# Performance work log

Measured on AMD Instinct MI355X. Metric: run time of the kernel, lower is better.

Reference implementation:

```python
import jax, jax.numpy as jnp
import numpy as np

NG, K, LEN_KEEP = 128, 32, 32  # n_groups, group_size, int(128*(1-0.75))
ENC_HEADS, DEC_HEADS = 12, 16


def _fps(xyz, init, npoint):
    # iterative farthest point sampling; xyz (B,N,3), init (B,) start indices
    B, N, _ = xyz.shape
    def step(carry, _):
        dmin, far = carry
        c = jnp.take_along_axis(xyz, far[:, None, None], axis=1)  # (B,1,3)
        dmin = jnp.minimum(dmin, jnp.sum((xyz - c) ** 2, -1))
        return (dmin, jnp.argmax(dmin, -1)), far
    _, cents = jax.lax.scan(step, (jnp.full((B, N), 1e10, xyz.dtype), init), None, length=npoint)
    return cents.T  # (B, npoint)


def _knn(xyz, cents, k):
    # squared-distance knn (same ordering as euclidean cdist + topk smallest)
    x2 = jnp.sum(xyz * xyz, -1)          # (B,N)
    c2 = jnp.sum(cents * cents, -1)      # (B,M)
    d = c2[:, :, None] + x2[:, None, :] - 2.0 * jnp.einsum('bmc,bnc->bmn', cents, xyz)
    idx = jax.lax.top_k(-d, k)[1]        # (B,M,k)
    return jax.vmap(lambda p, i: p[i])(xyz, idx)  # (B,M,k,3)


def _bn(x, g, b):
    # train-mode BatchNorm1d over (batch, spatial), channel-last x (BM,k,C)
    m = x.mean((0, 1))
    v = x.var((0, 1))
    return (x - m) * jax.lax.rsqrt(v + 1e-5) * g + b


def _ln(x, g, b):
    m = x.mean(-1, keepdims=True)
    v = ((x - m) ** 2).mean(-1, keepdims=True)
    return (x - m) * jax.lax.rsqrt(v + 1e-5) * g + b


def _layer(x, qw, qb, ow, ob, l1g, l1b, f1w, f1b, f2w, f2b, l2g, l2b, nh):
    # post-norm TransformerEncoderLayer (relu FFN, no dropout = eval mode)
    B, S, D = x.shape
    dh = D // nh
    q, k, v = jnp.split(x @ qw.T + qb, 3, axis=-1)
    q = q.reshape(B, S, nh, dh); k = k.reshape(B, S, nh, dh); v = v.reshape(B, S, nh, dh)
    att = jax.nn.softmax(jnp.einsum('bqhd,bkhd->bhqk', q, k) * (1.0 / float(np.sqrt(dh))), axis=-1)
    o = jnp.einsum('bhqk,bkhd->bqhd', att, v).reshape(B, S, D) @ ow.T + ob
    x = _ln(x + o, l1g, l1b)
    f = jax.nn.relu(x @ f1w.T + f1b) @ f2w.T + f2b
    return _ln(x + f, l2g, l2b)


def _stack(x, qw, qb, ow, ob, l1g, l1b, f1w, f1b, f2w, f2b, l2g, l2b, nh):
    for i in range(qw.shape[0]):
        x = _layer(x, qw[i], qb[i], ow[i], ob[i], l1g[i], l1b[i], f1w[i], f1b[i], f2w[i], f2b[i], l2g[i], l2b[i], nh)
    return x


def _forward(xyz, fps_init, ids_shuffle, cw1, cb1, g1, be1, cw2, cb2, g2, be2, cw3, cb3, g3, be3, pos_w, pos_b, eqw, eqb, eow, eob, el1g, el1b, ef1w, ef1b, ef2w, ef2b, el2g, el2b, dew, deb, mtok, dpw, dpb, dqw, dqb, dow, dob, dl1g, dl1b, df1w, df1b, df2w, df2b, dl2g, dl2b, prw, prb):
    B = xyz.shape[0]
    cent_idx = _fps(xyz, fps_init, NG)
    cxyz = jax.vmap(lambda p, i: p[i])(xyz, cent_idx)      # (B,NG,3)
    gn = _knn(xyz, cxyz, K) - cxyz[:, :, None, :]          # (B,NG,K,3) centered groups
    h = gn.reshape(-1, K, 3)
    h = jax.nn.relu(_bn(h @ cw1.T + cb1, g1, be1))
    h = jax.nn.relu(_bn(h @ cw2.T + cb2, g2, be2))
    h = _bn(h @ cw3.T + cb3, g3, be3)
    tokens = h.max(axis=1).reshape(B, NG, -1)              # (B,NG,768)
    x = tokens + cxyz @ pos_w.T + pos_b
    ids_restore = jnp.argsort(ids_shuffle, axis=1)
    xk = jnp.take_along_axis(x, ids_shuffle[:, :LEN_KEEP, None], axis=1)
    mask = jnp.ones((B, NG), xyz.dtype).at[:, :LEN_KEEP].set(0.0)
    mask = jnp.take_along_axis(mask, ids_restore, axis=1)
    lat = _stack(xk, eqw, eqb, eow, eob, el1g, el1b, ef1w, ef1b, ef2w, ef2b, el2g, el2b, ENC_HEADS)
    y = lat @ dew.T + deb
    mt = jnp.broadcast_to(mtok, (B, NG - LEN_KEEP, mtok.shape[0]))
    y_ = jnp.take_along_axis(jnp.concatenate([y, mt], axis=1), ids_restore[:, :, None], axis=1)
    yd = y_ + cxyz @ dpw.T + dpb
    dec = _stack(yd, dqw, dqb, dow, dob, dl1g, dl1b, df1w, df1b, df2w, df2b, dl2g, dl2b, DEC_HEADS)
    pred = dec @ prw.T + prb                               # (B,NG,K*3)
    target = gn.reshape(B, NG, -1)                         # same FPS seed -> same centroids in loss branch
    l = ((pred - target) ** 2).mean(-1)
    loss = (l * mask).sum() / mask.sum()
    return loss, pred, mask


def setup_inputs():
    ks = iter(jax.random.split(jax.random.key(0), 64))
    def W(*shape):
        return jax.random.normal(next(ks), shape, jnp.float32) * 0.02
    B, N, D, DD, Le, Ld = 32, 8192, 768, 512, 12, 8
    d = {}
    d['xyz'] = jax.random.normal(next(ks), (B, N, 3), jnp.float32)
    d['fps_init'] = jax.random.randint(next(ks), (B,), 0, N)
    d['ids_shuffle'] = jnp.argsort(jax.random.uniform(next(ks), (B, NG)), axis=1)
    d['cw1'], d['cb1'], d['g1'], d['be1'] = W(64, 3), jnp.zeros(64), jnp.ones(64), jnp.zeros(64)
    d['cw2'], d['cb2'], d['g2'], d['be2'] = W(128, 64), jnp.zeros(128), jnp.ones(128), jnp.zeros(128)
    d['cw3'], d['cb3'], d['g3'], d['be3'] = W(D, 128), jnp.zeros(D), jnp.ones(D), jnp.zeros(D)
    d['pos_w'], d['pos_b'] = W(D, 3), jnp.zeros(D)
    d['eqw'], d['eqb'] = W(Le, 3 * D, D), jnp.zeros((Le, 3 * D))
    d['eow'], d['eob'] = W(Le, D, D), jnp.zeros((Le, D))
    d['el1g'], d['el1b'] = jnp.ones((Le, D)), jnp.zeros((Le, D))
    d['ef1w'], d['ef1b'] = W(Le, 4 * D, D), jnp.zeros((Le, 4 * D))
    d['ef2w'], d['ef2b'] = W(Le, D, 4 * D), jnp.zeros((Le, D))
    d['el2g'], d['el2b'] = jnp.ones((Le, D)), jnp.zeros((Le, D))
    d['dew'], d['deb'] = W(DD, D), jnp.zeros(DD)
    d['mtok'] = jnp.zeros(DD)
    d['dpw'], d['dpb'] = W(DD, 3), jnp.zeros(DD)
    d['dqw'], d['dqb'] = W(Ld, 3 * DD, DD), jnp.zeros((Ld, 3 * DD))
    d['dow'], d['dob'] = W(Ld, DD, DD), jnp.zeros((Ld, DD))
    d['dl1g'], d['dl1b'] = jnp.ones((Ld, DD)), jnp.zeros((Ld, DD))
    d['df1w'], d['df1b'] = W(Ld, 4 * DD, DD), jnp.zeros((Ld, 4 * DD))
    d['df2w'], d['df2b'] = W(Ld, DD, 4 * DD), jnp.zeros((Ld, DD))
    d['dl2g'], d['dl2b'] = jnp.ones((Ld, DD)), jnp.zeros((Ld, DD))
    d['prw'], d['prb'] = W(K * 3, DD), jnp.zeros(K * 3)
    return d


def reference(xyz, fps_init, ids_shuffle, cw1, cb1, g1, be1, cw2, cb2, g2, be2, cw3, cb3, g3, be3, pos_w, pos_b, eqw, eqb, eow, eob, el1g, el1b, ef1w, ef1b, ef2w, ef2b, el2g, el2b, dew, deb, mtok, dpw, dpb, dqw, dqb, dow, dob, dl1g, dl1b, df1w, df1b, df2w, df2b, dl2g, dl2b, prw, prb):
    return _forward(xyz, fps_init, ids_shuffle, cw1, cb1, g1, be1, cw2, cb2, g2, be2, cw3, cb3, g3, be3, pos_w, pos_b, eqw, eqb, eow, eob, el1g, el1b, ef1w, ef1b, ef2w, ef2b, el2g, el2b, dew, deb, mtok, dpw, dpb, dqw, dqb, dow, dob, dl1g, dl1b, df1w, df1b, df2w, df2b, dl2g, dl2b, prw, prb)
```

## Files before the change

### kernel.cpp

```cpp
#include <hip/hip_runtime.h>
#include <cmath>

#define BB 32
#define NPTS 8192
#define NG 128
#define KNB 32
#define LK 32
#define DE 768
#define DD 512
#define NLE 12
#define NLD 8

typedef __bf16 bf16x8 __attribute__((ext_vector_type(8)));
typedef float  f32x4  __attribute__((ext_vector_type(4)));
typedef unsigned long long u64;

#define WAITV(N) asm volatile("s_waitcnt vmcnt(" #N ")" ::: "memory")

static __device__ __forceinline__ bf16x8 pack8(float4 a, float4 b) {
    bf16x8 h;
    h[0] = (__bf16)a.x; h[1] = (__bf16)a.y; h[2] = (__bf16)a.z; h[3] = (__bf16)a.w;
    h[4] = (__bf16)b.x; h[5] = (__bf16)b.y; h[6] = (__bf16)b.z; h[7] = (__bf16)b.w;
    return h;
}

static __device__ __forceinline__ void gload16(const __bf16* g, __bf16* l) {
    __builtin_amdgcn_global_load_lds(
        (const __attribute__((address_space(1))) void*)g,
        (__attribute__((address_space(3))) void*)l,
        16, 0, 0);
}

static __device__ __forceinline__ unsigned fkey(float f) {
    unsigned u = __float_as_uint(f);
    return ((int)u < 0) ? ~u : (u | 0x80000000u);
}

__global__ __launch_bounds__(256, 1) void fps_kernel(
    const float* __restrict__ xyz, const int* __restrict__ init,
    float* __restrict__ cxyz)
{
#pragma clang fp contract(off)
    const int b = blockIdx.x;
    const float* P = xyz + (size_t)b * NPTS * 3;
    __shared__ float pxs[NPTS], pys[NPTS], pzs[NPTS];
    __shared__ u64 red[2][4];
    const int tid = threadIdx.x;
    float x[32], y[32], z[32], dmin[32];
    #pragma unroll
    for (int k = 0; k < 32; ++k) {
        int n = tid + (k << 8);
        float xx = P[n * 3 + 0], yy = P[n * 3 + 1], zz = P[n * 3 + 2];
        x[k] = xx; y[k] = yy; z[k] = zz;
        pxs[n] = xx; pys[n] = yy; pzs[n] = zz;
        dmin[k] = 1e10f;
    }
    int far = init[b];
    __syncthreads();
    for (int t = 0; t < NG; ++t) {
        float cx = pxs[far], cy = pys[far], cz = pzs[far];
        if (tid == 0) {
            cxyz[(b * NG + t) * 3 + 0] = cx;
            cxyz[(b * NG + t) * 3 + 1] = cy;
            cxyz[(b * NG + t) * 3 + 2] = cz;
        }
        u64 key = 0ull;
        #pragma unroll
        for (int k = 0; k < 32; ++k) {
            float dx = x[k] - cx, dy = y[k] - cy, dz = z[k] - cz;
            float d = dx * dx + dy * dy + dz * dz;
            float dm = dmin[k];
            if (d < dm) dm = d;
            dmin[k] = dm;
            u64 kk = ((u64)__float_as_uint(dm) << 32) | (unsigned)(8191 - (tid + (k << 8)));
            if (kk > key) key = kk;
        }
        #pragma unroll
        for (int d = 32; d >= 1; d >>= 1) {
            u64 k2 = __shfl_down(key, d);
            if (k2 > key) key = k2;
        }
        if ((tid & 63) == 0) red[t & 1][tid >> 6] = key;
        __syncthreads();
        u64 kb = red[t & 1][0];
        #pragma unroll
        for (int w = 1; w < 4; ++w) {
            u64 k2 = red[t & 1][w];
            if (k2 > kb) kb = k2;
        }
        far = 8191 - (int)(kb & 0xFFFFFFFFu);
    }
}

__global__ __launch_bounds__(256) void knn_kernel(
    const float* __restrict__ xyz, const float* __restrict__ cxyz,
    float* __restrict__ gn)
{
#pragma clang fp contract(off)
    const int bm = blockIdx.x;
    const int b = bm / NG;
    const float* P = xyz + (size_t)b * NPTS * 3;
    __shared__ u64 cand[128];
    __shared__ int order[KNB];
    const int tid = threadIdx.x;
    const int wv = tid >> 6, lane = tid & 63;
    const float cx = cxyz[bm * 3 + 0], cy = cxyz[bm * 3 + 1], cz = cxyz[bm * 3 + 2];
    const float c2 = cx * cx + cy * cy + cz * cz;
    float d[32];
    float best = 1e31f; int bi = 1 << 30;
    #pragma unroll
    for (int j = 0; j < 32; ++j) {
        int n = tid + (j << 8);
        float x = P[n * 3 + 0], y = P[n * 3 + 1], z = P[n * 3 + 2];
        float x2 = x * x + y * y + z * z;
        float dt = cx * x + cy * y + cz * z;
        float v = (c2 + x2) - 2.0f * dt;
        d[j] = v;
        if (v < best) { best = v; bi = n; }
    }
    for (int r = 0; r < KNB; ++r) {
        float v = best; int i = bi;
        #pragma unroll
        for (int dd = 32; dd >= 1; dd >>= 1) {
            float v2 = __shfl_down(v, dd); int i2 = __shfl_down(i, dd);
            if (v2 < v || (v2 == v && i2 < i)) { v = v2; i = i2; }
        }
        v = __shfl(v, 0); i = __shfl(i, 0);
        if (lane == 0)
            cand[wv * 32 + r] = ((u64)fkey(v) << 32) | (unsigned)i;
        if ((i & 255) == tid) {
            int sj = i >> 8;
            best = 1e31f; bi = 1 << 30;
            #pragma unroll
            for (int j = 0; j < 32; ++j) {
                float vv = (j == sj) ? 1e30f : d[j];
                d[j] = vv;
                if (vv < best) { best = vv; bi = tid + (j << 8); }
            }
        }
    }
    __syncthreads();
    if (wv == 0) {
        u64 my0 = cand[lane], my1 = cand[lane + 64];
        int r0 = 0, r1 = 0;
        #pragma unroll 16
        for (int j = 0; j < 128; ++j) {
            u64 k = cand[j];
            r0 += (k < my0); r1 += (k < my1);
        }
        if (r0 < KNB) order[r0] = (int)(my0 & 0xFFFFFFFFu);
        if (r1 < KNB) order[r1] = (int)(my1 & 0xFFFFFFFFu);
    }
    __syncthreads();
    if (tid < KNB) {
        int n = order[tid];
        gn[((size_t)bm * KNB + tid) * 3 + 0] = P[n * 3 + 0] - cx;
        gn[((size_t)bm * KNB + tid) * 3 + 1] = P[n * 3 + 1] - cy;
        gn[((size_t)bm * KNB + tid) * 3 + 2] = P[n * 3 + 2] - cz;
    }
}

__global__ void cvt_bf16_kernel(const float* __restrict__ src, __bf16* __restrict__ dst, int n8)
{
    int i = blockIdx.x * 256 + threadIdx.x;
    if (i >= n8) return;
    const float4* p = (const float4*)(src + (size_t)i * 8);
    *(bf16x8*)(dst + (size_t)i * 8) = pack8(p[0], p[1]);
}

__global__ void embed1_kernel(const float* __restrict__ gn, const float* __restrict__ w,
                              const float* __restrict__ bias, float* __restrict__ h1)
{
    int i = blockIdx.x * 256 + threadIdx.x;
    if (i >= 131072 * 64) return;
    int r = i >> 6, c = i & 63;
    const float* p = gn + (size_t)r * 3;
    h1[i] = p[0] * w[c * 3 + 0] + p[1] * w[c * 3 + 1] + p[2] * w[c * 3 + 2] + bias[c];
}

template <int C>
__global__ __launch_bounds__(256) void colstats_kernel(const float* __restrict__ X,
                                                       double* __restrict__ st, int Mrows)
{
    constexpr int RL = 256 / C;
    const int c = threadIdx.x % C;
    const int rl = threadIdx.x / C;
    double s = 0.0, s2 = 0.0;
    int rows_per_block = (Mrows + gridDim.x - 1) / gridDim.x;
    int r0 = blockIdx.x * rows_per_block;
    int r1 = min(r0 + rows_per_block, Mrows);
    for (int r = r0 + rl; r < r1; r += RL) {
        float v = X[(size_t)r * C + c];
        s += v; s2 += (double)v * v;
    }
    __shared__ double sh[2][256];
    sh[0][threadIdx.x] = s; sh[1][threadIdx.x] = s2;
    __syncthreads();
    if (rl == 0) {
        for (int j = 1; j < RL; ++j) { s += sh[0][j * C + c]; s2 += sh[1][j * C + c]; }
        atomicAdd(&st[c], s);
        atomicAdd(&st[C + c], s2);
    }
}

__global__ void bn_finalize(const double* __restrict__ st, const float* __restrict__ g,
                            const float* __restrict__ be, float* __restrict__ sc,
                            float* __restrict__ shb, int C)
{
    int c = blockIdx.x * 64 + threadIdx.x;
    if (c >= C) return;
    double m = st[c] / 131072.0;
    double var = st[C + c] / 131072.0 - m * m;
    if (var < 0.0) var = 0.0;
    float rs = rsqrtf((float)var + 1e-5f);
    sc[c] = rs * g[c];
    shb[c] = be[c] - (float)m * rs * g[c];
}

__global__ void bn_apply_bf16(const float* __restrict__ x, const float* __restrict__ sc,
                              const float* __restrict__ shb, __bf16* __restrict__ y,
                              int total, int C)
{
    int i = blockIdx.x * 256 + threadIdx.x;
    if (i >= total) return;
    int c = i % C;
    float v = x[i] * sc[c] + shb[c];
    v = fmaxf(v, 0.0f);
    y[i] = (__bf16)v;
}

template <int BM, int WM, int WN, int DEPTH>
__global__ __launch_bounds__(256) void gemm_bf16(
    const __bf16* __restrict__ A, const __bf16* __restrict__ W,
    const float* __restrict__ bias, float* __restrict__ Cf, __bf16* __restrict__ Cb,
    int M, int N, int K, int Kc, int relu)
{
    constexpr int MR = BM / WM / 16;
    constexpr int NR = 128 / WN / 16;
    constexpr int CA = BM * 8 / 256;
    __shared__ __bf16 As[DEPTH][BM * 64];
    __shared__ __bf16 Ws[DEPTH][128 * 64];
    const int tid = threadIdx.x;
    const int lane = tid & 63;
    const int wave = tid >> 6;
    const int wm = wave / WN, wn = wave % WN;
    const int m0 = blockIdx.y * BM, n0 = blockIdx.x * 128;
    const int kb = blockIdx.z * Kc;

    f32x4 acc[MR][NR] = {};

    auto stage = [&](int buf, int kt) {
        #pragma unroll
        for (int j = 0; j < CA; ++j) {
            int cb = j * 256 + (wave << 6);
            int c  = cb + lane;
            int row = c >> 3;
            int kcs = (c & 7) ^ (row & 7);
            gload16(A + (size_t)(m0 + row) * K + kb + kt + kcs * 8, &As[buf][cb * 8]);
        }
        #pragma unroll
        for (int j = 0; j < 4; ++j) {
            int cb = j * 256 + (wave << 6);
            int c  = cb + lane;
            int row = c >> 3;
            int kcs = (c & 7) ^ (row & 7);
            gload16(W + (size_t)(n0 + row) * K + kb + kt + kcs * 8, &Ws[buf][cb * 8]);
        }
    };
    auto compute = [&](int buf) {
        #pragma unroll
        for (int ks = 0; ks < 2; ++ks) {
            bf16x8 af[MR], bfr[NR];
            int kc = ks * 4 + (lane >> 4);
            #pragma unroll
            for (int i = 0; i < MR; ++i) {
                int rowA = wm * (BM / WM) + i * 16 + (lane & 15);
                af[i] = *(bf16x8*)&As[buf][rowA * 64 + ((kc ^ (rowA & 7)) * 8)];
            }
            #pragma unroll
            for (int j = 0; j < NR; ++j) {
                int rowB = wn * (128 / WN) + j * 16 + (lane & 15);
                bfr[j] = *(bf16x8*)&Ws[buf][rowB * 64 + ((kc ^ (rowB & 7)) * 8)];
            }
            #pragma unroll
            for (int i = 0; i < MR; ++i)
                #pragma unroll
                for (int j = 0; j < NR; ++j)
                    acc[i][j] = __builtin_amdgcn_mfma_f32_16x16x32_bf16(af[i], bfr[j], acc[i][j], 0, 0, 0);
        }
    };

    const int nt = Kc >> 6;
    if constexpr (DEPTH == 3) {
        stage(0, 0);
        if (nt > 1) stage(1, 64);
        for (int t = 0; t < nt; ++t) {
            if (t < nt - 1) { if constexpr (BM == 64) WAITV(6); else WAITV(8); }
            else            WAITV(0);
            __syncthreads();
            if (t + 2 < nt) stage((t + 2) % 3, (t + 2) << 6);
            compute(t % 3);
        }
    } else {
        stage(0, 0);
        if (nt > 1) stage(1, 64);
        for (int t = 0; t < nt; ++t) {
            if (t < nt - 1) { if constexpr (BM == 64) WAITV(6); else WAITV(8); }
            else            WAITV(0);
            __syncthreads();
            compute(t % 2);
            if (t + 2 <= nt - 1) {
                __syncthreads();
                stage(t % 2, (t + 2) << 6);
            }
        }
    }

    float* Co = Cf ? Cf + (size_t)blockIdx.z * M * N : nullptr;
    #pragma unroll
    for (int j = 0; j < NR; ++j) {
        int col = n0 + wn * (128 / WN) + j * 16 + (lane & 15);
        if (col >= N) continue;
        float bv = (blockIdx.z == 0) ? bias[col] : 0.0f;
        #pragma unroll
        for (int i = 0; i < MR; ++i) {
            #pragma unroll
            for (int r = 0; r < 4; ++r) {
                int rowm = m0 + wm * (BM / WM) + i * 16 + (lane >> 4) * 4 + r;
                float v = acc[i][j][r] + bv;
                if (relu) v = fmaxf(v, 0.0f);
                if (Co) Co[(size_t)rowm * N + col] = v;
                if (Cb) Cb[(size_t)rowm * N + col] = (__bf16)v;
            }
        }
    }
}

__global__ __launch_bounds__(256) void embed3_mfma(
    const __bf16* __restrict__ A, const __bf16* __restrict__ W,
    const float* __restrict__ cb3,
    float* __restrict__ gmax, float* __restrict__ gmin, double* __restrict__ st3)
{
    __shared__ __bf16 As[2][128 * 64];
    __shared__ __bf16 Ws[2][128 * 64];
    const int tid = threadIdx.x;
    const int lane = tid & 63;
    const int wave = tid >> 6;
    const int wm = wave >> 1, wn = wave & 1;
    const int m0 = blockIdx.y * 128, n0 = blockIdx.x * 128;
    const int K = 128;

    f32x4 acc[4][4] = {};

    auto stage = [&](int buf, int kt) {
        #pragma unroll
        for (int j = 0; j < 4; ++j) {
            int cb = j * 256 + (wave << 6);
            int c  = cb + lane;
            int row = c >> 3;
            int kcs = (c & 7) ^ (row & 7);
            gload16(A + (size_t)(m0 + row) * K + kt + kcs * 8, &As[buf][cb * 8]);
            gload16(W + (size_t)(n0 + row) * K + kt + kcs * 8, &Ws[buf][cb * 8]);
        }
    };
    auto compute = [&](int buf) {
        #pragma unroll
        for (int ks = 0; ks < 2; ++ks) {
            bf16x8 af[4], bfr[4];
            int kc = ks * 4 + (lane >> 4);
            #pragma unroll
            for (int i = 0; i < 4; ++i) {
                int rowA = wm * 64 + i * 16 + (lane & 15);
                af[i] = *(bf16x8*)&As[buf][rowA * 64 + ((kc ^ (rowA & 7)) * 8)];
                int rowB = wn * 64 + i * 16 + (lane & 15);
                bfr[i] = *(bf16x8*)&Ws[buf][rowB * 64 + ((kc ^ (rowB & 7)) * 8)];
            }
            #pragma unroll
            for (int i = 0; i < 4; ++i)
                #pragma unroll
                for (int j = 0; j < 4; ++j)
                    acc[i][j] = __builtin_amdgcn_mfma_f32_16x16x32_bf16(af[i], bfr[j], acc[i][j], 0, 0, 0);
        }
    };

    stage(0, 0);
    stage(1, 64);
    WAITV(8);
    __syncthreads();
    compute(0);
    WAITV(0);
    __syncthreads();
    compute(1);

    #pragma unroll
    for (int j = 0; j < 4; ++j) {
        int col = n0 + wn * 64 + j * 16 + (lane & 15);
        float bv = cb3[col];
        float stot = 0.0f, s2tot = 0.0f;
        #pragma unroll
        for (int gi = 0; gi < 2; ++gi) {
            float mx = -1e30f, mn = 1e30f, s = 0.0f, s2 = 0.0f;
            #pragma unroll
            for (int ii = 0; ii < 2; ++ii) {
                f32x4 a = acc[gi * 2 + ii][j];
                #pragma unroll
                for (int r = 0; r < 4; ++r) {
                    float v = a[r] + bv;
                    mx = fmaxf(mx, v); mn = fminf(mn, v);
                    s += v; s2 += v * v;
                }
            }
            #pragma unroll
            for (int d = 16; d < 64; d <<= 1) {
                mx = fmaxf(mx, __shfl_xor(mx, d));
                mn = fminf(mn, __shfl_xor(mn, d));
                s  += __shfl_xor(s, d);
                s2 += __shfl_xor(s2, d);
            }
            stot += s; s2tot += s2;
            if (lane < 16) {
                int g = (m0 >> 5) + wm * 2 + gi;
                gmax[(size_t)g * 768 + col] = mx;
                gmin[(size_t)g * 768 + col] = mn;
            }
        }
        if (lane < 16) {
            double* stp = st3 + (size_t)(blockIdx.y & 31) * 1536;
            atomicAdd(&stp[col], (double)stot);
            atomicAdd(&stp[768 + col], (double)s2tot);
        }
    }
}

__global__ void bn3_finalize(const double* __restrict__ st3, const float* __restrict__ g,
                             const float* __restrict__ be, float* __restrict__ a3,
                             float* __restrict__ c3)
{
    int c = blockIdx.x * 256 + threadIdx.x;
    if (c >= 768) return;
    double s = 0.0, s2 = 0.0;
    for (int p = 0; p < 32; ++p) { s += st3[(size_t)p * 1536 + c]; s2 += st3[(size_t)p * 1536 + 768 + c]; }
    double m = s / 131072.0;
    double var = s2 / 131072.0 - m * m;
    if (var < 0.0) var = 0.0;
    float rs = rsqrtf((float)var + 1e-5f);
    a3[c] = rs * g[c];
    c3[c] = be[c] - (float)m * rs * g[c];
}

__global__ void tokens_pos(const float* __restrict__ gmax, const float* __restrict__ gmin,
                           const float* __restrict__ a3, const float* __restrict__ c3,
                           const float* __restrict__ cxyz, const float* __restrict__ posw,
                           const float* __restrict__ posb, float* __restrict__ x)
{
    int i = blockIdx.x * 256 + threadIdx.x;
    if (i >= 4096 * 768) return;
    int c = i % 768, g = i / 768;
    float a = a3[c];
    float tok = (a >= 0.0f ? a * gmax[i] : a * gmin[i]) + c3[c];
    float px = cxyz[g * 3 + 0], py = cxyz[g * 3 + 1], pz = cxyz[g * 3 + 2];
    x[i] = tok + px * posw[c * 3 + 0] + py * posw[c * 3 + 1] + pz * posw[c * 3 + 2] + posb[c];
}

__global__ void restore_kernel(const int* __restrict__ shuffle, int* __restrict__ restore,
                               float* __restrict__ maskv)
{
    int j = blockIdx.x * 256 + threadIdx.x;
    if (j >= BB * NG) return;
    int b = j / NG, p = j % NG;
    int dst = b * NG + shuffle[j];
    restore[dst] = p;
    maskv[dst] = (p < LK) ? 0.0f : 1.0f;
}

__global__ void gather_xk(const float* __restrict__ xfull, const int* __restrict__ shuffle,
                          float* __restrict__ xe, __bf16* __restrict__ xeb)
{
    int i = blockIdx.x * 256 + threadIdx.x;
    if (i >= BB * LK * DE) return;
    int c = i % DE;
    int s = (i / DE) % LK;
    int b = i / (DE * LK);
    float v = xfull[((size_t)b * NG + shuffle[b * NG + s]) * DE + c];
    xe[i] = v;
    xeb[i] = (__bf16)v;
}

__global__ void yd_build(const float* __restrict__ ykp, const int* __restrict__ restore,
                         const float* __restrict__ mtok, const float* __restrict__ cxyz,
                         const float* __restrict__ dpw, const float* __restrict__ dpb,
                         float* __restrict__ xd, __bf16* __restrict__ xdb)
{
    const size_t PS = (size_t)1024 * DD;
    int i = blockIdx.x * 256 + threadIdx.x;
    if (i >= BB * NG * DD) return;
    int c = i % DD;
    int g = i / DD;
    int b = g / NG;
    int r = restore[g];
    float base;
    if (r < LK) {
        size_t o = (size_t)(b * LK + r) * DD + c;
        base = ykp[o] + ykp[PS + o] + ykp[2 * PS + o] + ykp[3 * PS + o];
    } else {
        base = mtok[c];
    }
    float px = cxyz[g * 3 + 0], py = cxyz[g * 3 + 1], pz = cxyz[g * 3 + 2];
    float v = base + px * dpw[c * 3 + 0] + py * dpw[c * 3 + 1] + pz * dpw[c * 3 + 2] + dpb[c];
    xd[i] = v;
    xdb[i] = (__bf16)v;
}

template <int S, int DH, int QT, int NH>
__global__ __launch_bounds__(256) void attn_kernel(const float* __restrict__ qkv,
                                                   __bf16* __restrict__ o, float scale)
{
    constexpr int D = NH * DH;
    constexpr int NT = S / QT;
    constexpr int DH4 = DH / 4;
    constexpr int KW = DH + 4;
    constexpr int PS = S + 4;
    constexpr int CH = S / 8;
    __shared__ float Ks[S][KW];
    __shared__ float Vs[S][KW];
    __shared__ float Qs[QT][KW];
    __shared__ float Pb[QT][PS];
    const int t = blockIdx.x % NT;
    const int h = (blockIdx.x / NT) % NH;
    const int b = blockIdx.x / (NT * NH);
    const float* base = qkv + (size_t)b * S * 3 * D + h * DH;
    for (int i = threadIdx.x; i < S * DH4; i += 256) {
        int s = i / DH4, d4 = (i % DH4) * 4;
        *(float4*)&Ks[s][d4] = *(const float4*)&base[(size_t)s * 3 * D + D + d4];
        *(float4*)&Vs[s][d4] = *(const float4*)&base[(size_t)s * 3 * D + 2 * D + d4];
    }
    for (int i = threadIdx.x; i < QT * DH4; i += 256) {
        int qi = i / DH4, d4 = (i % DH4) * 4;
        *(float4*)&Qs[qi][d4] = *(const float4*)&base[(size_t)(t * QT + qi) * 3 * D + d4];
    }
    __syncthreads();
    for (int i = threadIdx.x; i < QT * S; i += 256) {
        int qi = i / S, s = i % S;
        float acc = 0.0f;
        #pragma unroll
        for (int d4 = 0; d4 < DH; d4 += 4) {
            float4 q = *(float4*)&Qs[qi][d4];
            float4 k = *(float4*)&Ks[s][d4];
            acc += q.x * k.x + q.y * k.y + q.z * k.z + q.w * k.w;
        }
        Pb[qi][s] = acc * scale;
    }
    __syncthreads();
    {
        int qi = threadIdx.x >> 3;
        int sub = threadIdx.x & 7;
        float mx = -1e30f;
        #pragma unroll
        for (int j = 0; j < CH; ++j) mx = fmaxf(mx, Pb[qi][sub * CH + j]);
        #pragma unroll
        for (int d = 4; d >= 1; d >>= 1) mx = fmaxf(mx, __shfl_xor(mx, d));
        float sum = 0.0f;
        #pragma unroll
        for (int j = 0; j < CH; ++j) {
            float e = expf(Pb[qi][sub * CH + j] - mx);
            Pb[qi][sub * CH + j] = e;
            sum += e;
        }
        #pragma unroll
        for (int d = 4; d >= 1; d >>= 1) sum += __shfl_xor(sum, d);
        float inv = 1.0f / sum;
        #pragma unroll
        for (int j = 0; j < CH; ++j) Pb[qi][sub * CH + j] *= inv;
    }
    __syncthreads();
    __bf16* ob = o + (size_t)b * S * D + h * DH;
    for (int i = threadIdx.x; i < QT * DH4; i += 256) {
        int qi = i / DH4, d4 = (i % DH4) * 4;
        float4 acc = {0, 0, 0, 0};
        for (int s = 0; s < S; ++s) {
            float p = Pb[qi][s];
            float4 v = *(float4*)&Vs[s][d4];
            acc.x += p * v.x; acc.y += p * v.y; acc.z += p * v.z; acc.w += p * v.w;
        }
        __bf16 o4[4] = {(__bf16)acc.x, (__bf16)acc.y, (__bf16)acc.z, (__bf16)acc.w};
        *(ushort4*)&ob[(size_t)(t * QT + qi) * D + d4] = *(ushort4*)o4;
    }
}

template <int D, int SK>
__global__ __launch_bounds__(256) void ln_res(float* __restrict__ x, const float* __restrict__ part,
                                              size_t pstride,
                                              const float* __restrict__ g, const float* __restrict__ b,
                                              __bf16* __restrict__ xb)
{
    constexpr int J = D / 256;
    __shared__ float pr[2][4];
    const size_t off = (size_t)blockIdx.x * D;
    const int tid = threadIdx.x;
    float vals[J];
    float s = 0.0f, s2 = 0.0f;
    #pragma unroll
    for (int j = 0; j < J; ++j) {
        int i = tid + j * 256;
        float v = x[off + i];
        #pragma unroll
        for (int sk = 0; sk < SK; ++sk) v += part[(size_t)sk * pstride + off + i];
        vals[j] = v; s += v; s2 += v * v;
    }
    #pragma unroll
    for (int d = 32; d >= 1; d >>= 1) { s += __shfl_down(s, d); s2 += __shfl_down(s2, d); }
    if ((tid & 63) == 0) { pr[0][tid >> 6] = s; pr[1][tid >> 6] = s2; }
    __syncthreads();
    float st = pr[0][0] + pr[0][1] + pr[0][2] + pr[0][3];
    float s2t = pr[1][0] + pr[1][1] + pr[1][2] + pr[1][3];
    float m = st / D;
    float var = s2t / D - m * m;
    if (var < 0.0f) var = 0.0f;
    float rs = rsqrtf(var + 1e-5f);
    #pragma unroll
    for (int j = 0; j < J; ++j) {
        int i = tid + j * 256;
        float v = (vals[j] - m) * rs * g[i] + b[i];
        x[off + i] = v;
        xb[off + i] = (__bf16)v;
    }
}

__global__ __launch_bounds__(128) void loss_l(const float* __restrict__ pred,
                                              const float* __restrict__ target,
                                              const float* __restrict__ maskv,
                                              float* __restrict__ lm)
{
    const int g = blockIdx.x;
    __shared__ float red[128];
    int t = threadIdx.x;
    float s = 0.0f;
    if (t < 96) {
        float d = pred[(size_t)g * 96 + t] - target[(size_t)g * 96 + t];
        s = d * d;
    }
    red[t] = s; __syncthreads();
    for (int st = 64; st > 0; st >>= 1) { if (t < st) red[t] += red[t + st]; __syncthreads(); }
    if (t == 0) lm[g] = (red[0] / 96.0f) * maskv[g];
}

__global__ __launch_bounds__(1024) void loss_final(const float* __restrict__ lm,
                                                   const float* __restrict__ maskv,
                                                   float* __restrict__ out)
{
    __shared__ float r1[1024], r2[1024];
    int t = threadIdx.x;
    float a = 0.0f, b = 0.0f;
    for (int i = t; i < BB * NG; i += 1024) { a += lm[i]; b += maskv[i]; }
    r1[t] = a; r2[t] = b; __syncthreads();
    for (int st = 512; st > 0; st >>= 1) { if (t < st) { r1[t] += r1[t + st]; r2[t] += r2[t + st]; } __syncthreads(); }
    if (t == 0) out[0] = r1[0] / r2[0];
}

extern "C" void kernel_launch(void* const* d_in, const int* in_sizes, int n_in,
                              void* d_out, int out_size, void* d_ws, size_t ws_size,
                              hipStream_t stream)
{
    (void)in_sizes; (void)n_in; (void)out_size; (void)ws_size;
    const float* xyz        = (const float*)d_in[0];
    const int*   fps_init   = (const int*)d_in[1];
    const int*   ids_shuf   = (const int*)d_in[2];
    const float* cw1 = (const float*)d_in[3];  const float* cb1 = (const float*)d_in[4];
    const float* g1  = (const float*)d_in[5];  const float* be1 = (const float*)d_in[6];
    const float* cw2 = (const float*)d_in[7];  const float* cb2 = (const float*)d_in[8];
    const float* g2  = (const float*)d_in[9];  const float* be2 = (const float*)d_in[10];
    const float* cw3 = (const float*)d_in[11]; const float* cb3 = (const float*)d_in[12];
    const float* g3  = (const float*)d_in[13]; const float* be3 = (const float*)d_in[14];
    const float* posw = (const float*)d_in[15]; const float* posb = (const float*)d_in[16];
    const float* eqw = (const float*)d_in[17]; const float* eqb = (const float*)d_in[18];
    const float* eow = (const float*)d_in[19]; const float* eob = (const float*)d_in[20];
    const float* el1g = (const float*)d_in[21]; const float* el1b = (const float*)d_in[22];
    const float* ef1w = (const float*)d_in[23]; const float* ef1b = (const float*)d_in[24];
    const float* ef2w = (const float*)d_in[25]; const float* ef2b = (const float*)d_in[26];
    const float* el2g = (const float*)d_in[27]; const float* el2b = (const float*)d_in[28];
    const float* dew = (const float*)d_in[29]; const float* deb = (const float*)d_in[30];
    const float* mtok = (const float*)d_in[31];
    const float* dpw = (const float*)d_in[32]; const float* dpb = (const float*)d_in[33];
    const float* dqw = (const float*)d_in[34]; const float* dqb = (const float*)d_in[35];
    const float* dow = (const float*)d_in[36]; const float* dob = (const float*)d_in[37];
    const float* dl1g = (const float*)d_in[38]; const float* dl1b = (const float*)d_in[39];
    const float* df1w = (const float*)d_in[40]; const float* df1b = (const float*)d_in[41];
    const float* df2w = (const float*)d_in[42]; const float* df2b = (const float*)d_in[43];
    const float* dl2g = (const float*)d_in[44]; const float* dl2b = (const float*)d_in[45];
    const float* prw = (const float*)d_in[46]; const float* prb = (const float*)d_in[47];
    float* out = (float*)d_out;
    float* pred = out + 1;
    float* maskv = out + 1 + (size_t)BB * NG * KNB * 3;

    char* ws = (char*)d_ws;
    size_t off = 0;
    auto alloc = [&](size_t bytes) -> void* {
        void* p = ws + off;
        off = (off + bytes + 255) & ~(size_t)255;
        return p;
    };
    double* st1 = (double*)alloc(128 * 8);
    double* st2 = (double*)alloc(256 * 8);
    double* st3 = (double*)alloc((size_t)32 * 1536 * 8);
    float* sc1 = (float*)alloc(64 * 4);  float* sh1 = (float*)alloc(64 * 4);
    float* sc2 = (float*)alloc(128 * 4); float* sh2 = (float*)alloc(128 * 4);
    float* a3 = (float*)alloc(768 * 4);  float* c3 = (float*)alloc(768 * 4);
    int* restore = (int*)alloc(4096 * 4);
    float* cxyz = (float*)alloc(12288 * 4);
    float* gn   = (float*)alloc((size_t)393216 * 4);
    __bf16* cw2b = (__bf16*)alloc((size_t)128 * 64 * 2);
    __bf16* cw3b = (__bf16*)alloc((size_t)768 * 128 * 2);
    float* xfull = (float*)alloc((size_t)4096 * 768 * 4);
    float* xe    = (float*)alloc((size_t)1024 * 768 * 4);
    __bf16* xeb  = (__bf16*)alloc((size_t)1024 * 768 * 2);
    float* qkve  = (float*)alloc((size_t)1024 * 2304 * 4);
    __bf16* oeb  = (__bf16*)alloc((size_t)1024 * 768 * 2);
    __bf16* fe1b = (__bf16*)alloc((size_t)1024 * 3072 * 2);
    float* xd    = (float*)alloc((size_t)4096 * 512 * 4);
    __bf16* xdb  = (__bf16*)alloc((size_t)4096 * 512 * 2);
    float* qkvd  = (float*)alloc((size_t)4096 * 1536 * 4);
    __bf16* odb  = (__bf16*)alloc((size_t)4096 * 512 * 2);
    __bf16* fd1b = (__bf16*)alloc((size_t)4096 * 2048 * 2);
    float* lm    = (float*)alloc(4096 * 4);

    __bf16* eqwb  = (__bf16*)alloc((size_t)NLE * 3 * DE * DE * 2);
    __bf16* eowb  = (__bf16*)alloc((size_t)NLE * DE * DE * 2);
    __bf16* ef1wb = (__bf16*)alloc((size_t)NLE * 4 * DE * DE * 2);
    __bf16* ef2wb = (__bf16*)alloc((size_t)NLE * 4 * DE * DE * 2);
    __bf16* dewb  = (__bf16*)alloc((size_t)DD * DE * 2);
    __bf16* dqwb  = (__bf16*)alloc((size_t)NLD * 3 * DD * DD * 2);
    __bf16* dowb  = (__bf16*)alloc((size_t)NLD * DD * DD * 2);
    __bf16* df1wb = (__bf16*)alloc((size_t)NLD * 4 * DD * DD * 2);
    __bf16* df2wb = (__bf16*)alloc((size_t)NLD * 4 * DD * DD * 2);
    __bf16* prwb  = (__bf16*)alloc((size_t)128 * 512 * 2);

    char* U = (char*)eqwb;
    float*  h1   = (float*)U;
    __bf16* h1b  = (__bf16*)(U + (size_t)33554432);
    float*  h2   = (float*)(U + (size_t)50331648);
    __bf16* h2b  = (__bf16*)(U + (size_t)117440512);
    float*  gmax = (float*)(U + (size_t)150994944);
    float*  gmin = (float*)(U + (size_t)163577856);

    size_t stats_bytes = (size_t)((char*)st3 + (size_t)32 * 1536 * 8 - (char*)st1);
    hipMemsetAsync((void*)st1, 0, stats_bytes, stream);

    auto cvt = [&](const float* src, __bf16* dst, size_t n) {
        int n8 = (int)(n / 8);
        cvt_bf16_kernel<<<(n8 + 255) / 256, 256, 0, stream>>>(src, dst, n8);
    };
    auto gemm = [&](const __bf16* A, const __bf16* Wt, const float* bias,
                    float* Cf, __bf16* Cb, int M, int N, int K, int relu) {
        int nb128 = ((N + 127) / 128) * (M / 128);
        if (nb128 < 256) {
            dim3 grid((N + 127) / 128, M / 64, 1);
            gemm_bf16<64, 1, 4, 3><<<grid, 256, 0, stream>>>(A, Wt, bias, Cf, Cb, M, N, K, K, relu);
        } else {
            dim3 grid((N + 127) / 128, M / 128, 1);
            gemm_bf16<128, 2, 2, 2><<<grid, 256, 0, stream>>>(A, Wt, bias, Cf, Cb, M, N, K, K, relu);
        }
    };
    auto gemmSK = [&](const __bf16* A, const __bf16* Wt, const float* bias,
                      float* Cf, int M, int N, int K, int SK) {
        dim3 grid((N + 127) / 128, M / 64, SK);
        gemm_bf16<64, 1, 4, 3><<<grid, 256, 0, stream>>>(A, Wt, bias, Cf, nullptr, M, N, K, K / SK, 0);
    };

    cvt(cw2, cw2b, 128 * 64);
    cvt(cw3, cw3b, 768 * 128);

    fps_kernel<<<BB, 256, 0, stream>>>(xyz, fps_init, cxyz);
    knn_kernel<<<BB * NG, 256, 0, stream>>>(xyz, cxyz, gn);

    embed1_kernel<<<(131072 * 64 + 255) / 256, 256, 0, stream>>>(gn, cw1, cb1, h1);
    colstats_kernel<64><<<256, 256, 0, stream>>>(h1, st1, 131072);
    bn_finalize<<<1, 64, 0, stream>>>(st1, g1, be1, sc1, sh1, 64);
    bn_apply_bf16<<<(131072 * 64 + 255) / 256, 256, 0, stream>>>(h1, sc1, sh1, h1b, 131072 * 64, 64);
    gemm(h1b, cw2b, cb2, h2, nullptr, 131072, 128, 64, 0);
    colstats_kernel<128><<<256, 256, 0, stream>>>(h2, st2, 131072);
    bn_finalize<<<2, 64, 0, stream>>>(st2, g2, be2, sc2, sh2, 128);
    bn_apply_bf16<<<(131072 * 128 + 255) / 256, 256, 0, stream>>>(h2, sc2, sh2, h2b, 131072 * 128, 128);
    embed3_mfma<<<dim3(6, 1024), 256, 0, stream>>>(h2b, cw3b, cb3, gmax, gmin, st3);
    bn3_finalize<<<3, 256, 0, stream>>>(st3, g3, be3, a3, c3);
    tokens_pos<<<(4096 * 768 + 255) / 256, 256, 0, stream>>>(gmax, gmin, a3, c3, cxyz, posw, posb, xfull);

    restore_kernel<<<16, 256, 0, stream>>>(ids_shuf, restore, maskv);
    gather_xk<<<(BB * LK * DE + 255) / 256, 256, 0, stream>>>(xfull, ids_shuf, xe, xeb);

    cvt(eqw,  eqwb,  (size_t)NLE * 3 * DE * DE);
    cvt(eow,  eowb,  (size_t)NLE * DE * DE);
    cvt(ef1w, ef1wb, (size_t)NLE * 4 * DE * DE);
    cvt(ef2w, ef2wb, (size_t)NLE * 4 * DE * DE);
    cvt(dew,  dewb,  (size_t)DD * DE);
    cvt(dqw,  dqwb,  (size_t)NLD * 3 * DD * DD);
    cvt(dow,  dowb,  (size_t)NLD * DD * DD);
    cvt(df1w, df1wb, (size_t)NLD * 4 * DD * DD);
    cvt(df2w, df2wb, (size_t)NLD * 4 * DD * DD);
    cvt(prw,  prwb,  (size_t)96 * 512);
    hipMemsetAsync((void*)(prwb + (size_t)96 * 512), 0, (size_t)32 * 512 * 2, stream);

    const size_t PSE = (size_t)1024 * DE;
    const size_t PSD = (size_t)4096 * DD;

    for (int l = 0; l < NLE; ++l) {
        gemm(xeb, eqwb + (size_t)l * 3 * DE * DE, eqb + (size_t)l * 3 * DE, qkve, nullptr, 1024, 3 * DE, DE, 0);
        attn_kernel<LK, 64, 32, 12><<<BB * 12, 256, 0, stream>>>(qkve, oeb, 0.125f);
        gemmSK(oeb, eowb + (size_t)l * DE * DE, eob + (size_t)l * DE, xfull, 1024, DE, DE, 4);
        ln_res<DE, 4><<<BB * LK, 256, 0, stream>>>(xe, xfull, PSE, el1g + (size_t)l * DE, el1b + (size_t)l * DE, xeb);
        gemm(xeb, ef1wb + (size_t)l * 4 * DE * DE, ef1b + (size_t)l * 4 * DE, nullptr, fe1b, 1024, 4 * DE, DE, 1);
        gemmSK(fe1b, ef2wb + (size_t)l * DE * 4 * DE, ef2b + (size_t)l * DE, xfull, 1024, DE, 4 * DE, 4);
        ln_res<DE, 4><<<BB * LK, 256, 0, stream>>>(xe, xfull, PSE, el2g + (size_t)l * DE, el2b + (size_t)l * DE, xeb);
    }

    gemmSK(xeb, dewb, deb, qkve, 1024, DD, DE, 4);
    yd_build<<<(BB * NG * DD + 255) / 256, 256, 0, stream>>>(qkve, restore, mtok, cxyz, dpw, dpb, xd, xdb);

    const float dsc = (float)(1.0 / sqrt(32.0));
    for (int l = 0; l < NLD; ++l) {
        gemm(xdb, dqwb + (size_t)l * 3 * DD * DD, dqb + (size_t)l * 3 * DD, qkvd, nullptr, 4096, 3 * DD, DD, 0);
        attn_kernel<NG, 32, 32, 16><<<BB * 16 * (NG / 32), 256, 0, stream>>>(qkvd, odb, dsc);
        gemmSK(odb, dowb + (size_t)l * DD * DD, dob + (size_t)l * DD, qkvd, 4096, DD, DD, 2);
        ln_res<DD, 2><<<BB * NG, 256, 0, stream>>>(xd, qkvd, PSD, dl1g + (size_t)l * DD, dl1b + (size_t)l * DD, xdb);
        gemm(xdb, df1wb + (size_t)l * 4 * DD * DD, df1b + (size_t)l * 4 * DD, nullptr, fd1b, 4096, 4 * DD, DD, 1);
        gemmSK(fd1b, df2wb + (size_t)l * DD * 4 * DD, df2b + (size_t)l * DD, qkvd, 4096, DD, 4 * DD, 2);
        ln_res<DD, 2><<<BB * NG, 256, 0, stream>>>(xd, qkvd, PSD, dl2g + (size_t)l * DD, dl2b + (size_t)l * DD, xdb);
    }

    gemm(xdb, prwb, prb, pred, nullptr, 4096, 96, 512, 0);
    loss_l<<<BB * NG, 128, 0, stream>>>(pred, gn, maskv, lm);
    loss_final<<<1, 1024, 0, stream>>>(lm, maskv, out);
}
```

Baseline: 2.779 ms.

## Replace iterative kNN selection with threshold filter plus rank sort; batch weight casts

The kNN kernel no longer runs 32 rounds of wavefront argmin. Each wave bitonic-sorts its per-thread minima to get the 32nd smallest as a threshold, and all candidates at or below the tightest wave threshold are compacted into shared memory and rank-sorted. If more than 512 candidates pass, it falls back to a block-wide iterative selection. The ten separate fp32-to-bf16 weight conversion launches are also merged into one segmented kernel, which cuts launch overhead but adds a per-thread segment lookup.

```diff
diff --git a/kernel.cpp b/kernel.cpp
--- a/kernel.cpp
+++ b/kernel.cpp
@@ -100,14 +100,16 @@
     const int bm = blockIdx.x;
     const int b = bm / NG;
     const float* P = xyz + (size_t)b * NPTS * 3;
-    __shared__ u64 cand[128];
+    __shared__ u64 cand[512];
+    __shared__ u64 tmins[4];
+    __shared__ int wcnt[4];
     __shared__ int order[KNB];
     const int tid = threadIdx.x;
     const int wv = tid >> 6, lane = tid & 63;
     const float cx = cxyz[bm * 3 + 0], cy = cxyz[bm * 3 + 1], cz = cxyz[bm * 3 + 2];
     const float c2 = cx * cx + cy * cy + cz * cz;
-    float d[32];
-    float best = 1e31f; int bi = 1 << 30;
+    unsigned fk[32];
+    float bestf = 1e31f; int bi = 1 << 30;
     #pragma unroll
     for (int j = 0; j < 32; ++j) {
         int n = tid + (j << 8);
@@ -115,43 +117,99 @@
         float x2 = x * x + y * y + z * z;
         float dt = cx * x + cy * y + cz * z;
         float v = (c2 + x2) - 2.0f * dt;
-        d[j] = v;
-        if (v < best) { best = v; bi = n; }
-    }
-    for (int r = 0; r < KNB; ++r) {
-        float v = best; int i = bi;
-        #pragma unroll
-        for (int dd = 32; dd >= 1; dd >>= 1) {
-            float v2 = __shfl_down(v, dd); int i2 = __shfl_down(i, dd);
-            if (v2 < v || (v2 == v && i2 < i)) { v = v2; i = i2; }
-        }
-        v = __shfl(v, 0); i = __shfl(i, 0);
-        if (lane == 0)
-            cand[wv * 32 + r] = ((u64)fkey(v) << 32) | (unsigned)i;
-        if ((i & 255) == tid) {
-            int sj = i >> 8;
-            best = 1e31f; bi = 1 << 30;
-            #pragma unroll
-            for (int j = 0; j < 32; ++j) {
-                float vv = (j == sj) ? 1e30f : d[j];
-                d[j] = vv;
-                if (vv < best) { best = vv; bi = tid + (j << 8); }
-            }
-        }
+        fk[j] = fkey(v);
+        if (v < bestf) { bestf = v; bi = n; }
+    }
+    u64 mk = ((u64)fkey(bestf) << 32) | (unsigned)bi;
+    {
+        u64 v = mk;
+        #pragma unroll
+        for (int k = 2; k <= 64; k <<= 1) {
+            #pragma unroll
+            for (int j = k >> 1; j > 0; j >>= 1) {
+                u64 o = __shfl_xor(v, j);
+                bool up = ((lane & k) == 0);
+                bool lower = ((lane & j) == 0);
+                u64 mn = (v < o) ? v : o;
+                u64 mx = (v < o) ? o : v;
+                v = (up == lower) ? mn : mx;
+            }
+        }
+        u64 Tw = __shfl(v, 31);
+        if (lane == 0) tmins[wv] = Tw;
     }
     __syncthreads();
-    if (wv == 0) {
-        u64 my0 = cand[lane], my1 = cand[lane + 64];
-        int r0 = 0, r1 = 0;
-        #pragma unroll 16
-        for (int j = 0; j < 128; ++j) {
-            u64 k = cand[j];
-            r0 += (k < my0); r1 += (k < my1);
-        }
-        if (r0 < KNB) order[r0] = (int)(my0 & 0xFFFFFFFFu);
-        if (r1 < KNB) order[r1] = (int)(my1 & 0xFFFFFFFFu);
-    }
+    u64 T = tmins[0];
+    #pragma unroll
+    for (int w = 1; w < 4; ++w) { u64 k2 = tmins[w]; if (k2 < T) T = k2; }
+    int c = 0;
+    #pragma unroll
+    for (int j = 0; j < 32; ++j) {
+        u64 key = ((u64)fk[j] << 32) | (unsigned)(tid + (j << 8));
+        c += (key <= T) ? 1 : 0;
+    }
+    int s = c;
+    #pragma unroll
+    for (int d = 1; d < 64; d <<= 1) {
+        int t2 = __shfl_up(s, d);
+        if (lane >= d) s += t2;
+    }
+    int excl = s - c;
+    if (lane == 63) wcnt[wv] = s;
     __syncthreads();
+    int base = 0;
+    for (int w = 0; w < wv; ++w) base += wcnt[w];
+    int etot = wcnt[0] + wcnt[1] + wcnt[2] + wcnt[3];
+
+    if (etot <= 512) {
+        int pos = base + excl;
+        #pragma unroll
+        for (int j = 0; j < 32; ++j) {
+            u64 key = ((u64)fk[j] << 32) | (unsigned)(tid + (j << 8));
+            if (key <= T) cand[pos++] = key;
+        }
+        __syncthreads();
+        for (int si = tid; si < etot; si += 256) {
+            u64 my = cand[si];
+            int r = 0;
+            for (int j2 = 0; j2 < etot; ++j2) r += (cand[j2] < my) ? 1 : 0;
+            if (r < KNB) order[r] = (int)(my & 0xFFFFFFFFu);
+        }
+        __syncthreads();
+    } else {
+        u64 bk = ~0ull;
+        #pragma unroll
+        for (int j = 0; j < 32; ++j) {
+            u64 key = ((u64)fk[j] << 32) | (unsigned)(tid + (j << 8));
+            if (key < bk) bk = key;
+        }
+        for (int r = 0; r < KNB; ++r) {
+            u64 kk = bk;
+            #pragma unroll
+            for (int dd = 32; dd >= 1; dd >>= 1) {
+                u64 k2 = __shfl_down(kk, dd);
+                if (k2 < kk) kk = k2;
+            }
+            if (lane == 0) cand[(r & 1) * 4 + wv] = kk;
+            __syncthreads();
+            u64 kb = cand[(r & 1) * 4 + 0];
+            #pragma unroll
+            for (int w = 1; w < 4; ++w) { u64 k2 = cand[(r & 1) * 4 + w]; if (k2 < kb) kb = k2; }
+            if (tid == 0) order[r] = (int)(kb & 0xFFFFFFFFu);
+            if ((int)(kb & 255u) == tid) {
+                int sj = (int)((kb & 0xFFFFFFFFu) >> 8);
+                #pragma unroll
+                for (int j = 0; j < 32; ++j) if (j == sj) fk[j] = 0xFFFFFFFFu;
+                bk = ~0ull;
+                #pragma unroll
+                for (int j = 0; j < 32; ++j) {
+                    u64 key = ((u64)fk[j] << 32) | (unsigned)(tid + (j << 8));
+                    if (key < bk) bk = key;
+                }
+            }
+            __syncthreads();
+        }
+    }
     if (tid < KNB) {
         int n = order[tid];
         gn[((size_t)bm * KNB + tid) * 3 + 0] = P[n * 3 + 0] - cx;
@@ -166,6 +224,23 @@
     if (i >= n8) return;
     const float4* p = (const float4*)(src + (size_t)i * 8);
     *(bf16x8*)(dst + (size_t)i * 8) = pack8(p[0], p[1]);
+}
+
+struct CvtTab {
+    const float* src[10];
+    __bf16* dst[10];
+    int cum[11];
+};
+__global__ void cvt_multi_kernel(CvtTab t)
+{
+    int i = blockIdx.x * 256 + threadIdx.x;
+    if (i >= t.cum[10]) return;
+    int seg = 0;
+    #pragma unroll
+    for (int k = 1; k < 10; ++k) seg += (i >= t.cum[k]) ? 1 : 0;
+    int local = i - t.cum[seg];
+    const float4* p = (const float4*)(t.src[seg] + (size_t)local * 8);
+    *(bf16x8*)(t.dst[seg] + (size_t)local * 8) = pack8(p[0], p[1]);
 }
 
 __global__ void embed1_kernel(const float* __restrict__ gn, const float* __restrict__ w,
@@ -787,17 +862,28 @@
     restore_kernel<<<16, 256, 0, stream>>>(ids_shuf, restore, maskv);
     gather_xk<<<(BB * LK * DE + 255) / 256, 256, 0, stream>>>(xfull, ids_shuf, xe, xeb);
 
-    cvt(eqw,  eqwb,  (size_t)NLE * 3 * DE * DE);
-    cvt(eow,  eowb,  (size_t)NLE * DE * DE);
-    cvt(ef1w, ef1wb, (size_t)NLE * 4 * DE * DE);
-    cvt(ef2w, ef2wb, (size_t)NLE * 4 * DE * DE);
-    cvt(dew,  dewb,  (size_t)DD * DE);
-    cvt(dqw,  dqwb,  (size_t)NLD * 3 * DD * DD);
-    cvt(dow,  dowb,  (size_t)NLD * DD * DD);
-    cvt(df1w, df1wb, (size_t)NLD * 4 * DD * DD);
-    cvt(df2w, df2wb, (size_t)NLD * 4 * DD * DD);
-    cvt(prw,  prwb,  (size_t)96 * 512);
-    hipMemsetAsync((void*)(prwb + (size_t)96 * 512), 0, (size_t)32 * 512 * 2, stream);
+    {
+        CvtTab t;
+        const float* srcs[10] = {eqw, eow, ef1w, ef2w, dew, dqw, dow, df1w, df2w, prw};
+        __bf16* dsts[10] = {eqwb, eowb, ef1wb, ef2wb, dewb, dqwb, dowb, df1wb, df2wb, prwb};
+        size_t ns[10] = {
+            (size_t)NLE * 3 * DE * DE, (size_t)NLE * DE * DE,
+            (size_t)NLE * 4 * DE * DE, (size_t)NLE * 4 * DE * DE,
+            (size_t)DD * DE,
+            (size_t)NLD * 3 * DD * DD, (size_t)NLD * DD * DD,
+            (size_t)NLD * 4 * DD * DD, (size_t)NLD * 4 * DD * DD,
+            (size_t)96 * 512
+        };
+        int cum = 0;
+        t.cum[0] = 0;
+        for (int k = 0; k < 10; ++k) {
+            t.src[k] = srcs[k]; t.dst[k] = dsts[k];
+            cum += (int)(ns[k] / 8);
+            t.cum[k + 1] = cum;
+        }
+        cvt_multi_kernel<<<(cum + 255) / 256, 256, 0, stream>>>(t);
+        hipMemsetAsync((void*)(prwb + (size_t)96 * 512), 0, (size_t)32 * 512 * 2, stream);
+    }
 
     const size_t PSE = (size_t)1024 * DE;
     const size_t PSD = (size_t)4096 * DD;
```

After: 2.618 ms. -5.8%, faster.
